# Performance work log

Measured on AMD Instinct MI355X. Metric: run time of the kernel, lower is better.

## Reference

```python
import jax, jax.numpy as jnp
import numpy as np

DIM = 1024
EXP = 4
B, S = 4, 4096


def setup_inputs() -> dict:
    key = jax.random.key(0)
    ks = jax.random.split(key, 20)
    d, h = DIM, DIM * EXP
    sc = 1.0 / np.sqrt(d)
    inp = {
        "x": jax.random.normal(ks[0], (B, S, d), dtype=jnp.float32),
        # attention linears, stored [in, out] so y = x @ W + b
        "wq": jax.random.normal(ks[1], (d, d), jnp.float32) * sc,
        "bq": jnp.zeros((d,), jnp.float32),
        "wk": jax.random.normal(ks[2], (d, d), jnp.float32) * sc,
        "bk": jnp.zeros((d,), jnp.float32),
        "wv": jax.random.normal(ks[3], (d, d), jnp.float32) * sc,
        "bv": jnp.zeros((d,), jnp.float32),
        "wo": jax.random.normal(ks[4], (d, d), jnp.float32) * sc,
        "bo": jnp.zeros((d,), jnp.float32),
        # FFN
        "w1": jax.random.normal(ks[5], (d, h), jnp.float32) * sc,
        "b1": jnp.zeros((h,), jnp.float32),
        "w2": jax.random.normal(ks[6], (h, d), jnp.float32) * (1.0 / np.sqrt(h)),
        "b2": jnp.zeros((d,), jnp.float32),
        # LayerNorms
        "g1": jnp.ones((d,), jnp.float32),
        "beta1": jnp.zeros((d,), jnp.float32),
        "g2": jnp.ones((d,), jnp.float32),
        "beta2": jnp.zeros((d,), jnp.float32),
    }
    return inp


def _layernorm(x, g, b, eps=1e-5):
    mu = jnp.mean(x, axis=-1, keepdims=True)
    var = jnp.mean(jnp.square(x - mu), axis=-1, keepdims=True)
    return (x - mu) * jax.lax.rsqrt(var + eps) * g + b


def _block(x, wq, bq, wk, bk, wv, bv, wo, bo, w1, b1, w2, b2, g1, beta1, g2, beta2):
    d = x.shape[-1]
    # attention sub-block (single head, full [B,S,S] scores as in source)
    h = _layernorm(x, g1, beta1)
    q = h @ wq + bq
    k = h @ wk + bk
    v = h @ wv + bv
    scores = jnp.einsum("bsd,btd->bst", q, k) / jnp.sqrt(jnp.asarray(d, x.dtype))
    attn = jax.nn.softmax(scores, axis=-1)
    a = jnp.einsum("bst,btd->bsd", attn, v) @ wo + bo
    x = x + a
    # FFN sub-block (exact GELU, matching torch nn.GELU default)
    h2 = _layernorm(x, g2, beta2)
    f = jax.nn.gelu(h2 @ w1 + b1, approximate=False) @ w2 + b2
    return x + f


def reference(x, wq, bq, wk, bk, wv, bv, wo, bo, w1, b1, w2, b2, g1, beta1, g2, beta2):
    return _block(x, wq, bq, wk, bk, wv, bv, wo, bo, w1, b1, w2, b2, g1, beta1, g2, beta2)
```

## Files before the change

### kernel.cpp

```cpp
#include <hip/hip_runtime.h>
#include <hip/hip_bf16.h>
#include <cstdint>

typedef __bf16 bf16;
typedef __bf16 bf16x8 __attribute__((ext_vector_type(8)));
typedef __bf16 bf16x4 __attribute__((ext_vector_type(4)));
typedef float f32x4 __attribute__((ext_vector_type(4)));

#define DEV __device__ __forceinline__

DEV float wred_sum(float v) {
#pragma unroll
  for (int off = 32; off > 0; off >>= 1) v += __shfl_xor(v, off, 64);
  return v;
}
DEV float wred_max(float v) {
#pragma unroll
  for (int off = 32; off > 0; off >>= 1) v = fmaxf(v, __shfl_xor(v, off, 64));
  return v;
}

__global__ void convT_kernel(const float* __restrict__ in, bf16* __restrict__ out,
                             int K, int N) {
  __shared__ float t[32][33];
  const int n0 = blockIdx.x * 32, k0 = blockIdx.y * 32;
  const int tx = threadIdx.x & 31, ty = threadIdx.x >> 5;
#pragma unroll
  for (int i = 0; i < 4; i++)
    t[ty + 8 * i][tx] = in[(long)(k0 + ty + 8 * i) * N + n0 + tx];
  __syncthreads();
#pragma unroll
  for (int i = 0; i < 4; i++)
    out[(long)(n0 + ty + 8 * i) * K + k0 + tx] = (bf16)t[tx][ty + 8 * i];
}

__global__ void transpose_bf16(const bf16* __restrict__ in, bf16* __restrict__ out,
                               int ldin, int ldout) {
  __shared__ bf16 t[32][33];
  const int c0 = blockIdx.x * 32, r0 = blockIdx.y * 32;
  const int tx = threadIdx.x & 31, ty = threadIdx.x >> 5;
#pragma unroll
  for (int i = 0; i < 4; i++)
    t[ty + 8 * i][tx] = in[(long)(r0 + ty + 8 * i) * ldin + c0 + tx];
  __syncthreads();
#pragma unroll
  for (int i = 0; i < 4; i++)
    out[(long)(c0 + ty + 8 * i) * ldout + r0 + tx] = t[tx][ty + 8 * i];
}

__global__ void ln_bf16_kernel(const float* __restrict__ x, const float* __restrict__ g,
                               const float* __restrict__ be, bf16* __restrict__ out) {
  const long row = blockIdx.x;
  const int tid = threadIdx.x;
  const float4 v = ((const float4*)(x + row * 1024))[tid];
  float s = v.x + v.y + v.z + v.w;
  float s2 = v.x * v.x + v.y * v.y + v.z * v.z + v.w * v.w;
  __shared__ float rs_[4], rs2_[4];
  s = wred_sum(s);
  s2 = wred_sum(s2);
  const int wave = tid >> 6, lane = tid & 63;
  if (lane == 0) { rs_[wave] = s; rs2_[wave] = s2; }
  __syncthreads();
  s = rs_[0] + rs_[1] + rs_[2] + rs_[3];
  s2 = rs2_[0] + rs2_[1] + rs2_[2] + rs2_[3];
  const float mu = s * (1.0f / 1024.0f);
  const float var = s2 * (1.0f / 1024.0f) - mu * mu;
  const float rstd = rsqrtf(var + 1e-5f);
  const float4 gg = ((const float4*)g)[tid];
  const float4 bb = ((const float4*)be)[tid];
  bf16x4 o;
  o[0] = (bf16)((v.x - mu) * rstd * gg.x + bb.x);
  o[1] = (bf16)((v.y - mu) * rstd * gg.y + bb.y);
  o[2] = (bf16)((v.z - mu) * rstd * gg.z + bb.z);
  o[3] = (bf16)((v.w - mu) * rstd * gg.w + bb.w);
  *(bf16x4*)(out + row * 1024 + tid * 4) = o;
}

__global__ void softmax_kernel(bf16* __restrict__ p) {
  const long row = blockIdx.x;
  bf16* pr = p + row * 4096;
  const int tid = threadIdx.x;
  bf16x8 a = *(const bf16x8*)(pr + tid * 16);
  bf16x8 b = *(const bf16x8*)(pr + tid * 16 + 8);
  float v[16];
#pragma unroll
  for (int i = 0; i < 8; i++) { v[i] = (float)a[i]; v[8 + i] = (float)b[i]; }
  float mx = -1e30f;
#pragma unroll
  for (int i = 0; i < 16; i++) mx = fmaxf(mx, v[i]);
  __shared__ float red1[4], red2[4];
  mx = wred_max(mx);
  const int wave = tid >> 6, lane = tid & 63;
  if (lane == 0) red1[wave] = mx;
  __syncthreads();
  mx = fmaxf(fmaxf(red1[0], red1[1]), fmaxf(red1[2], red1[3]));
  float s = 0.0f;
#pragma unroll
  for (int i = 0; i < 16; i++) { v[i] = __expf(v[i] - mx); s += v[i]; }
  s = wred_sum(s);
  if (lane == 0) red2[wave] = s;
  __syncthreads();
  s = red2[0] + red2[1] + red2[2] + red2[3];
  const float inv = 1.0f / s;
#pragma unroll
  for (int i = 0; i < 8; i++) { a[i] = (bf16)(v[i] * inv); b[i] = (bf16)(v[8 + i] * inv); }
  *(bf16x8*)(pr + tid * 16) = a;
  *(bf16x8*)(pr + tid * 16 + 8) = b;
}

enum { EPI_BF16 = 0, EPI_QKV = 1, EPI_GELU = 2, EPI_F32RES = 3 };

DEV void stage16(const bf16* g, bf16* l) {
  __builtin_amdgcn_global_load_lds((const __attribute__((address_space(1))) void*)g,
                                   (__attribute__((address_space(3))) void*)l, 16, 0, 0);
}

template <int EPI>
__global__ __launch_bounds__(256)
void gemm128(const bf16* __restrict__ A, const bf16* __restrict__ B,
             const float* __restrict__ bias, const float* __restrict__ resid,
             void* Cout, int M, int N, int K,
             int lda, int ldb, int ldc, float alpha) {
  extern __shared__ __align__(16) char smem[];
  bf16* sA = (bf16*)smem;
  bf16* sB = sA + 4 * 8192;
  int flat = (int)(blockIdx.y * gridDim.x + blockIdx.x);
  {
    const int nwg = (int)(gridDim.x * gridDim.y);
    const int qq = nwg >> 3, rr = nwg & 7;
    const int xcd = flat & 7, idx = flat >> 3;
    flat = (xcd < rr ? xcd * (qq + 1) : rr * (qq + 1) + (xcd - rr) * qq) + idx;
  }
  const int bix = flat % (int)gridDim.x, biy = flat / (int)gridDim.x;
  const int tid = threadIdx.x;
  const int lane = tid & 63;
  const int wid = tid >> 6;
  const int q = lane >> 4, r16 = lane & 15;
  const int wr = wid >> 1, wc = wid & 1;
  const long m0 = (long)biy * 128;
  const long n0 = (long)bix * 128;
  const int srow = tid >> 3;
  const int gcol = ((tid & 7) ^ (srow & 7)) * 8;
  const long lda32 = (long)lda * 32, ldb32 = (long)ldb * 32;
  const bf16* Ag = A + (m0 + srow) * (long)lda + gcol;
  const bf16* Bg = B + (n0 + srow) * (long)ldb + gcol;
  const int NT = K >> 6;
  const int swz = r16 * 64 + ((q ^ (r16 & 7)) * 8);
  const int abase = wr * 4096 + swz;
  const int bbase = wc * 4096 + swz;
  f32x4 acc[4][4] = {};

  const int PRE = NT < 3 ? NT : 3;
  for (int tt = 0; tt < PRE; ++tt) {
#pragma unroll
    for (int blk = 0; blk < 4; ++blk) {
      stage16(Ag + tt * 64 + blk * lda32, sA + tt * 8192 + tid * 8 + blk * 2048);
      stage16(Bg + tt * 64 + blk * ldb32, sB + tt * 8192 + tid * 8 + blk * 2048);
    }
  }
  if (NT >= 3)      asm volatile("s_waitcnt vmcnt(16)" ::: "memory");
  else if (NT == 2) asm volatile("s_waitcnt vmcnt(8)" ::: "memory");
  else              asm volatile("s_waitcnt vmcnt(0)" ::: "memory");
  __builtin_amdgcn_sched_barrier(0);
  __builtin_amdgcn_s_barrier();
  __builtin_amdgcn_sched_barrier(0);

  for (int t = 0; t < NT; ++t) {
    const int bx = (t & 3) * 8192;
    if (t + 3 < NT) {
      const int bs = ((t + 3) & 3) * 8192;
      const bf16* Agn = Ag + (t + 3) * 64;
      const bf16* Bgn = Bg + (t + 3) * 64;
#pragma unroll
      for (int blk = 0; blk < 4; ++blk) {
        stage16(Agn + blk * lda32, sA + bs + tid * 8 + blk * 2048);
        stage16(Bgn + blk * ldb32, sB + bs + tid * 8 + blk * 2048);
      }
    }
    const bf16* sAb = sA + bx;
    const bf16* sBb = sB + bx;
    bf16x8 a0[4], a1[4], b0[4], b1[4];
#pragma unroll
    for (int i = 0; i < 4; ++i) {
      a0[i] = *(const bf16x8*)(sAb + (abase + i * 1024));
      a1[i] = *(const bf16x8*)(sAb + ((abase + i * 1024) ^ 32));
      b0[i] = *(const bf16x8*)(sBb + (bbase + i * 1024));
      b1[i] = *(const bf16x8*)(sBb + ((bbase + i * 1024) ^ 32));
    }
#pragma unroll
    for (int i = 0; i < 4; ++i)
#pragma unroll
      for (int j = 0; j < 4; ++j) {
        acc[i][j] = __builtin_amdgcn_mfma_f32_16x16x32_bf16(b0[j], a0[i], acc[i][j], 0, 0, 0);
        acc[i][j] = __builtin_amdgcn_mfma_f32_16x16x32_bf16(b1[j], a1[i], acc[i][j], 0, 0, 0);
      }
    if (t + 3 < NT)      asm volatile("s_waitcnt vmcnt(16)" ::: "memory");
    else if (t + 2 < NT) asm volatile("s_waitcnt vmcnt(8)" ::: "memory");
    else if (t + 1 < NT) asm volatile("s_waitcnt vmcnt(0)" ::: "memory");
    if (t + 1 < NT) {
      __builtin_amdgcn_sched_barrier(0);
      __builtin_amdgcn_s_barrier();
      __builtin_amdgcn_sched_barrier(0);
    }
  }

#pragma unroll
  for (int i = 0; i < 4; ++i) {
    const long row = m0 + wr * 64 + i * 16 + r16;
#pragma unroll
    for (int j = 0; j < 4; ++j) {
      const int ncol = (int)n0 + wc * 64 + j * 16 + q * 4;
      float4 b4 = make_float4(0.f, 0.f, 0.f, 0.f);
      if (bias != nullptr) b4 = *(const float4*)(bias + ncol);
      float v0 = acc[i][j][0] * alpha + b4.x;
      float v1 = acc[i][j][1] * alpha + b4.y;
      float v2 = acc[i][j][2] * alpha + b4.z;
      float v3 = acc[i][j][3] * alpha + b4.w;
      if (EPI == EPI_F32RES) {
        const long idx = row * (long)ldc + ncol;
        const float4 rr = *(const float4*)(resid + idx);
        const float4 o = make_float4(v0 + rr.x, v1 + rr.y, v2 + rr.z, v3 + rr.w);
        *(float4*)((float*)Cout + idx) = o;
      } else {
        bf16x4 o;
        o[0] = (bf16)v0; o[1] = (bf16)v1; o[2] = (bf16)v2; o[3] = (bf16)v3;
        *(bf16x4*)((bf16*)Cout + row * (long)ldc + ncol) = o;
      }
    }
  }
}

template <int EPI>
__global__ __launch_bounds__(512, 2)
void gemm256(const bf16* __restrict__ A, const bf16* __restrict__ B,
             const float* __restrict__ bias, const float* bias2, const float* bias3,
             const float* resid, void* Cout, int M, int N, int K,
             int lda, int ldb, int ldc, float alpha) {
  extern __shared__ __align__(16) char smem[];
  bf16* sA = (bf16*)smem;
  bf16* sB = sA + 32768;
  const int tid = threadIdx.x;
  const int lane = tid & 63;
  const int wid = tid >> 6;
  const int q = lane >> 4, r16 = lane & 15;
  const int wr = wid >> 2, wc = wid & 3;
  const long m0 = (long)blockIdx.y * 256;
  const long n0 = (long)blockIdx.x * 256;
  const int srow = tid >> 3;
  const int gcol = ((tid & 7) ^ (srow & 7)) * 8;
  const long lda64 = (long)lda * 64, ldb64 = (long)ldb * 64;
  const bf16* AgT = A + (m0 + srow) * (long)lda + gcol;
  const bf16* BgT = B + (n0 + srow) * (long)ldb + gcol;
  bf16* lA = sA + tid * 8;
  bf16* lB = sB + tid * 8;
  const int NT = K >> 6;
  const int swz = r16 * 64 + ((q ^ (r16 & 7)) * 8);
  const int abase = wr * 8192 + swz;
  const int bbase = (wc >> 1) * 8192 + (wc & 1) * 4096 + swz;

  f32x4 acc[8][4] = {};

  stage16(AgT,              lA);
  stage16(AgT + 2 * lda64,  lA + 8192);
  stage16(AgT + lda64,      lA + 4096);
  stage16(AgT + 3 * lda64,  lA + 12288);
  stage16(BgT,              lB);
  stage16(BgT + ldb64,      lB + 4096);
  stage16(BgT + 2 * ldb64,  lB + 8192);
  stage16(BgT + 3 * ldb64,  lB + 12288);
  if (NT > 1) {
    stage16(AgT + 64,             lA + 16384);
    stage16(AgT + 64 + 2 * lda64, lA + 16384 + 8192);
    stage16(BgT + 64,             lB + 16384);
    stage16(BgT + 64 + ldb64,     lB + 16384 + 4096);
    stage16(BgT + 64 + 2 * ldb64, lB + 16384 + 8192);
    stage16(BgT + 64 + 3 * ldb64, lB + 16384 + 12288);
    stage16(AgT + 64 + lda64,     lA + 16384 + 4096);
    stage16(AgT + 64 + 3 * lda64, lA + 16384 + 12288);
    asm volatile("s_waitcnt vmcnt(8)" ::: "memory");
  } else {
    asm volatile("s_waitcnt vmcnt(0)" ::: "memory");
  }
  __builtin_amdgcn_sched_barrier(0);
  __builtin_amdgcn_s_barrier();
  __builtin_amdgcn_sched_barrier(0);

  for (int t = 0; t < NT; ++t) {
    const int bx = (t & 1) * 16384;
    const int nbx = 16384 - bx;
    const bf16* sAb = sA + bx;
    const bf16* sBb = sB + bx;
    const long k1 = (long)(t + 1) * 64;
    const long k2 = (long)(t + 2) * 64;
    bf16x8 b0[4], b1[4];
#pragma unroll
    for (int p = 0; p < 4; ++p) {
      if (p == 0) {
#pragma unroll
        for (int n = 0; n < 4; ++n) {
          b0[n] = *(const bf16x8*)(sBb + (bbase + n * 1024));
          b1[n] = *(const bf16x8*)(sBb + ((bbase + n * 1024) ^ 32));
        }
      }
      const int ab = abase + p * 2048;
      const bf16x8 a00 = *(const bf16x8*)(sAb + ab);
      const bf16x8 a10 = *(const bf16x8*)(sAb + (ab ^ 32));
      const bf16x8 a01 = *(const bf16x8*)(sAb + (ab + 1024));
      const bf16x8 a11 = *(const bf16x8*)(sAb + ((ab + 1024) ^ 32));
      if (p == 0 && t >= 1 && t + 1 < NT) {
        stage16(AgT + k1 + lda64,     lA + nbx + 4096);
        stage16(AgT + k1 + 3 * lda64, lA + nbx + 12288);
      }
      if (p == 1 && t + 2 < NT) {
        stage16(BgT + k2,         lB + bx);
        stage16(BgT + k2 + ldb64, lB + bx + 4096);
      }
      if (p == 2 && t + 2 < NT) {
        stage16(AgT + k2,             lA + bx);
        stage16(AgT + k2 + 2 * lda64, lA + bx + 8192);
      }
      if (p == 3 && t + 2 < NT) {
        stage16(BgT + k2 + 2 * ldb64, lB + bx + 8192);
        stage16(BgT + k2 + 3 * ldb64, lB + bx + 12288);
      }
      __builtin_amdgcn_sched_barrier(0);
      __builtin_amdgcn_s_barrier();
      __builtin_amdgcn_sched_barrier(0);
      __builtin_amdgcn_s_setprio(1);
#pragma unroll
      for (int n = 0; n < 4; ++n) {
        acc[2 * p][n]     = __builtin_amdgcn_mfma_f32_16x16x32_bf16(b0[n], a00, acc[2 * p][n], 0, 0, 0);
        acc[2 * p][n]     = __builtin_amdgcn_mfma_f32_16x16x32_bf16(b1[n], a10, acc[2 * p][n], 0, 0, 0);
        acc[2 * p + 1][n] = __builtin_amdgcn_mfma_f32_16x16x32_bf16(b0[n], a01, acc[2 * p + 1][n], 0, 0, 0);
        acc[2 * p + 1][n] = __builtin_amdgcn_mfma_f32_16x16x32_bf16(b1[n], a11, acc[2 * p + 1][n], 0, 0, 0);
      }
      __builtin_amdgcn_s_setprio(0);
      if (p == 1) {
        if (t + 2 < NT)      asm volatile("s_waitcnt vmcnt(10)" ::: "memory");
        else if (t + 1 < NT) asm volatile("s_waitcnt vmcnt(8)" ::: "memory");
        else                 asm volatile("s_waitcnt vmcnt(0)" ::: "memory");
      }
      if (p == 3) {
        if (t + 2 < NT)      asm volatile("s_waitcnt vmcnt(8)" ::: "memory");
        else if (t + 1 < NT) asm volatile("s_waitcnt vmcnt(2)" ::: "memory");
      }
      __builtin_amdgcn_sched_barrier(0);
      __builtin_amdgcn_s_barrier();
      __builtin_amdgcn_sched_barrier(0);
    }
  }

#pragma unroll
  for (int m = 0; m < 8; ++m) {
    const long row = m0 + wr * 128 + m * 16 + r16;
#pragma unroll
    for (int n = 0; n < 4; ++n) {
      const int ncol = (int)n0 + wc * 64 + n * 16 + q * 4;
      float4 b4 = make_float4(0.f, 0.f, 0.f, 0.f);
      if (EPI == EPI_QKV) {
        const int band = ncol >> 10;
        const float* bsel = band == 0 ? bias : (band == 1 ? bias2 : bias3);
        b4 = *(const float4*)(bsel + (ncol & 1023));
      } else if (bias != nullptr) {
        b4 = *(const float4*)(bias + ncol);
      }
      float v0 = acc[m][n][0] * alpha + b4.x;
      float v1 = acc[m][n][1] * alpha + b4.y;
      float v2 = acc[m][n][2] * alpha + b4.z;
      float v3 = acc[m][n][3] * alpha + b4.w;
      if (EPI == EPI_GELU) {
        v0 = 0.5f * v0 * (1.0f + erff(v0 * 0.70710678118654752f));
        v1 = 0.5f * v1 * (1.0f + erff(v1 * 0.70710678118654752f));
        v2 = 0.5f * v2 * (1.0f + erff(v2 * 0.70710678118654752f));
        v3 = 0.5f * v3 * (1.0f + erff(v3 * 0.70710678118654752f));
      }
      if (EPI == EPI_F32RES) {
        const long idx = row * (long)ldc + ncol;
        const float4 rr = *(const float4*)(resid + idx);
        const float4 o = make_float4(v0 + rr.x, v1 + rr.y, v2 + rr.z, v3 + rr.w);
        *(float4*)((float*)Cout + idx) = o;
      } else {
        bf16x4 o;
        o[0] = (bf16)v0; o[1] = (bf16)v1; o[2] = (bf16)v2; o[3] = (bf16)v3;
        *(bf16x4*)((bf16*)Cout + row * (long)ldc + ncol) = o;
      }
    }
  }
}

extern "C" void kernel_launch(void* const* d_in, const int* in_sizes, int n_in,
                              void* d_out, int out_size, void* d_ws, size_t ws_size,
                              hipStream_t stream) {
  const float* x  = (const float*)d_in[0];
  const float* wq = (const float*)d_in[1];
  const float* bq = (const float*)d_in[2];
  const float* wk = (const float*)d_in[3];
  const float* bk = (const float*)d_in[4];
  const float* wv = (const float*)d_in[5];
  const float* bv = (const float*)d_in[6];
  const float* wo = (const float*)d_in[7];
  const float* bo = (const float*)d_in[8];
  const float* w1 = (const float*)d_in[9];
  const float* b1 = (const float*)d_in[10];
  const float* w2 = (const float*)d_in[11];
  const float* b2 = (const float*)d_in[12];
  const float* g1 = (const float*)d_in[13];
  const float* be1 = (const float*)d_in[14];
  const float* g2 = (const float*)d_in[15];
  const float* be2 = (const float*)d_in[16];

  static int attr_done = 0;
  if (!attr_done) {
    attr_done = 1;
    hipFuncSetAttribute(reinterpret_cast<const void*>(&gemm256<EPI_QKV>),
                        hipFuncAttributeMaxDynamicSharedMemorySize, 131072);
    hipFuncSetAttribute(reinterpret_cast<const void*>(&gemm256<EPI_BF16>),
                        hipFuncAttributeMaxDynamicSharedMemorySize, 131072);
    hipFuncSetAttribute(reinterpret_cast<const void*>(&gemm256<EPI_GELU>),
                        hipFuncAttributeMaxDynamicSharedMemorySize, 131072);
    hipFuncSetAttribute(reinterpret_cast<const void*>(&gemm256<EPI_F32RES>),
                        hipFuncAttributeMaxDynamicSharedMemorySize, 131072);
    hipFuncSetAttribute(reinterpret_cast<const void*>(&gemm128<EPI_BF16>),
                        hipFuncAttributeMaxDynamicSharedMemorySize, 131072);
    hipFuncSetAttribute(reinterpret_cast<const void*>(&gemm128<EPI_F32RES>),
                        hipFuncAttributeMaxDynamicSharedMemorySize, 131072);
  }

  const long MB = 1 << 20;
  char* ws = (char*)d_ws;
  char* ob = (char*)d_out;
  bf16* WQKV = (bf16*)(ws + 0 * MB);
  bf16* WO   = (bf16*)(ws + 6 * MB);
  bf16* W1   = (bf16*)(ws + 8 * MB);
  bf16* W2   = (bf16*)(ws + 16 * MB);
  bf16* H    = (bf16*)(ws + 24 * MB);
  bf16* P    = (bf16*)(ob + 0 * MB);
  bf16* QKVb = (bf16*)(ob + 32 * MB);
  bf16* Vt   = (bf16*)(ob + 56 * MB);
  float* OUT = (float*)d_out;
  const dim3 blk(256);
  const dim3 blk512(512);
  const size_t SMEM = 131072;
  const size_t SMEM128 = 131072;

  convT_kernel<<<dim3(32, 32), blk, 0, stream>>>(wq, WQKV, 1024, 1024);
  convT_kernel<<<dim3(32, 32), blk, 0, stream>>>(wk, WQKV + 1024 * 1024, 1024, 1024);
  convT_kernel<<<dim3(32, 32), blk, 0, stream>>>(wv, WQKV + 2048 * 1024, 1024, 1024);
  convT_kernel<<<dim3(32, 32), blk, 0, stream>>>(wo, WO, 1024, 1024);
  convT_kernel<<<dim3(128, 32), blk, 0, stream>>>(w1, W1, 1024, 4096);
  convT_kernel<<<dim3(32, 128), blk, 0, stream>>>(w2, W2, 4096, 1024);
  ln_bf16_kernel<<<16384, blk, 0, stream>>>(x, g1, be1, H);
  for (int z = 0; z < 4; z++) {
    const long zo = (long)z * 4096 * 1024;
    gemm256<EPI_QKV><<<dim3(12, 16), blk512, SMEM, stream>>>(
        H + zo, WQKV, bq, bk, bv, nullptr, QKVb,
        4096, 3072, 1024, 1024, 1024, 3072, 1.0f);
    transpose_bf16<<<dim3(32, 128), blk, 0, stream>>>(QKVb + 2048, Vt, 3072, 4096);
    gemm256<EPI_BF16><<<dim3(16, 16), blk512, SMEM, stream>>>(
        QKVb, QKVb + 1024, nullptr, nullptr, nullptr, nullptr, P,
        4096, 4096, 1024, 3072, 3072, 4096, 1.0f / 32.0f);
    softmax_kernel<<<4096, blk, 0, stream>>>(P);
    gemm128<EPI_BF16><<<dim3(8, 32), blk, SMEM128, stream>>>(
        P, Vt, nullptr, nullptr, H + zo,
        4096, 1024, 4096, 4096, 4096, 1024, 1.0f);
  }
  gemm256<EPI_F32RES><<<dim3(4, 64), blk512, SMEM, stream>>>(
      H, WO, bo, nullptr, nullptr, x, OUT,
      16384, 1024, 1024, 1024, 1024, 1024, 1.0f);
  bf16* H2m = (bf16*)(ws + 0 * MB);
  bf16* Fm  = (bf16*)(ws + 24 * MB);
  for (int mc = 0; mc < 4; mc++) {
    const long ro = (long)mc * 4096 * 1024;
    ln_bf16_kernel<<<4096, blk, 0, stream>>>(OUT + ro, g2, be2, H2m);
    gemm256<EPI_GELU><<<dim3(16, 16), blk512, SMEM, stream>>>(
        H2m, W1, b1, nullptr, nullptr, nullptr, Fm,
        4096, 4096, 1024, 1024, 1024, 4096, 1.0f);
    gemm128<EPI_F32RES><<<dim3(8, 32), blk, SMEM128, stream>>>(
        Fm, W2, b2, OUT + ro, OUT + ro,
        4096, 1024, 4096, 4096, 4096, 1024, 1.0f);
  }
  (void)in_sizes; (void)n_in; (void)out_size; (void)ws_size;
}
```

Measured before the change: 1.257 ms.

## Replace 128x128 GEMM with 64x128 tile, 3-stage ring, two blocks per CU

The 128x128 GEMM used for attn@V and the FFN down-projection becomes a 64x128 tile kernel. It uses a 3-stage LDS ring instead of 4 stages, needs 72KB of shared memory, and sets launch bounds for 2 blocks per CU. The grid doubles to 512 blocks to improve CU fill for the K=4096, N=1024 GEMMs, and MFMA sections get setprio. The change also drops sched_barrier fences around s_barrier in gemm256, which gives the compiler more freedom but risks reordering around the LDS pipeline.

```diff
diff --git a/kernel.cpp b/kernel.cpp
--- a/kernel.cpp
+++ b/kernel.cpp
@@ -115,29 +115,30 @@
                                    (__attribute__((address_space(3))) void*)l, 16, 0, 0);
 }
 
+DEV int xcd_swizzle(int flat, int nwg) {
+  const int qq = nwg >> 3, rr = nwg & 7;
+  const int xcd = flat & 7, idx = flat >> 3;
+  return (xcd < rr ? xcd * (qq + 1) : rr * (qq + 1) + (xcd - rr) * qq) + idx;
+}
+
 template <int EPI>
-__global__ __launch_bounds__(256)
-void gemm128(const bf16* __restrict__ A, const bf16* __restrict__ B,
-             const float* __restrict__ bias, const float* __restrict__ resid,
-             void* Cout, int M, int N, int K,
-             int lda, int ldb, int ldc, float alpha) {
+__global__ __launch_bounds__(256, 2)
+void gemm64(const bf16* __restrict__ A, const bf16* __restrict__ B,
+            const float* __restrict__ bias, const float* __restrict__ resid,
+            void* Cout, int M, int N, int K,
+            int lda, int ldb, int ldc, float alpha) {
   extern __shared__ __align__(16) char smem[];
   bf16* sA = (bf16*)smem;
-  bf16* sB = sA + 4 * 8192;
+  bf16* sB = sA + 3 * 4096;
   int flat = (int)(blockIdx.y * gridDim.x + blockIdx.x);
-  {
-    const int nwg = (int)(gridDim.x * gridDim.y);
-    const int qq = nwg >> 3, rr = nwg & 7;
-    const int xcd = flat & 7, idx = flat >> 3;
-    flat = (xcd < rr ? xcd * (qq + 1) : rr * (qq + 1) + (xcd - rr) * qq) + idx;
-  }
+  flat = xcd_swizzle(flat, (int)(gridDim.x * gridDim.y));
   const int bix = flat % (int)gridDim.x, biy = flat / (int)gridDim.x;
   const int tid = threadIdx.x;
   const int lane = tid & 63;
   const int wid = tid >> 6;
   const int q = lane >> 4, r16 = lane & 15;
   const int wr = wid >> 1, wc = wid & 1;
-  const long m0 = (long)biy * 128;
+  const long m0 = (long)biy * 64;
   const long n0 = (long)bix * 128;
   const int srow = tid >> 3;
   const int gcol = ((tid & 7) ^ (srow & 7)) * 8;
@@ -146,67 +147,70 @@
   const bf16* Bg = B + (n0 + srow) * (long)ldb + gcol;
   const int NT = K >> 6;
   const int swz = r16 * 64 + ((q ^ (r16 & 7)) * 8);
-  const int abase = wr * 4096 + swz;
+  const int abase = wr * 2048 + swz;
   const int bbase = wc * 4096 + swz;
-  f32x4 acc[4][4] = {};
-
-  const int PRE = NT < 3 ? NT : 3;
+  f32x4 acc[2][4] = {};
+
+  const int PRE = NT < 2 ? NT : 2;
   for (int tt = 0; tt < PRE; ++tt) {
 #pragma unroll
-    for (int blk = 0; blk < 4; ++blk) {
-      stage16(Ag + tt * 64 + blk * lda32, sA + tt * 8192 + tid * 8 + blk * 2048);
+    for (int blk = 0; blk < 2; ++blk)
+      stage16(Ag + tt * 64 + blk * lda32, sA + tt * 4096 + tid * 8 + blk * 2048);
+#pragma unroll
+    for (int blk = 0; blk < 4; ++blk)
       stage16(Bg + tt * 64 + blk * ldb32, sB + tt * 8192 + tid * 8 + blk * 2048);
-    }
-  }
-  if (NT >= 3)      asm volatile("s_waitcnt vmcnt(16)" ::: "memory");
-  else if (NT == 2) asm volatile("s_waitcnt vmcnt(8)" ::: "memory");
-  else              asm volatile("s_waitcnt vmcnt(0)" ::: "memory");
-  __builtin_amdgcn_sched_barrier(0);
+  }
+  if (NT >= 2) asm volatile("s_waitcnt vmcnt(6)" ::: "memory");
+  else         asm volatile("s_waitcnt vmcnt(0)" ::: "memory");
   __builtin_amdgcn_s_barrier();
-  __builtin_amdgcn_sched_barrier(0);
-
+
+  int bxA = 0, bxB = 0;
+  int bsA = 8192, bsB = 16384;
   for (int t = 0; t < NT; ++t) {
-    const int bx = (t & 3) * 8192;
-    if (t + 3 < NT) {
-      const int bs = ((t + 3) & 3) * 8192;
-      const bf16* Agn = Ag + (t + 3) * 64;
-      const bf16* Bgn = Bg + (t + 3) * 64;
-#pragma unroll
-      for (int blk = 0; blk < 4; ++blk) {
-        stage16(Agn + blk * lda32, sA + bs + tid * 8 + blk * 2048);
-        stage16(Bgn + blk * ldb32, sB + bs + tid * 8 + blk * 2048);
-      }
-    }
-    const bf16* sAb = sA + bx;
-    const bf16* sBb = sB + bx;
-    bf16x8 a0[4], a1[4], b0[4], b1[4];
-#pragma unroll
-    for (int i = 0; i < 4; ++i) {
+    if (t + 2 < NT) {
+      const bf16* Agn = Ag + (t + 2) * 64;
+      const bf16* Bgn = Bg + (t + 2) * 64;
+#pragma unroll
+      for (int blk = 0; blk < 2; ++blk)
+        stage16(Agn + blk * lda32, sA + bsA + tid * 8 + blk * 2048);
+#pragma unroll
+      for (int blk = 0; blk < 4; ++blk)
+        stage16(Bgn + blk * ldb32, sB + bsB + tid * 8 + blk * 2048);
+    }
+    const bf16* sAb = sA + bxA;
+    const bf16* sBb = sB + bxB;
+    bf16x8 a0[2], a1[2], b0[4], b1[4];
+#pragma unroll
+    for (int i = 0; i < 2; ++i) {
       a0[i] = *(const bf16x8*)(sAb + (abase + i * 1024));
       a1[i] = *(const bf16x8*)(sAb + ((abase + i * 1024) ^ 32));
-      b0[i] = *(const bf16x8*)(sBb + (bbase + i * 1024));
-      b1[i] = *(const bf16x8*)(sBb + ((bbase + i * 1024) ^ 32));
-    }
-#pragma unroll
-    for (int i = 0; i < 4; ++i)
+    }
+#pragma unroll
+    for (int j = 0; j < 4; ++j) {
+      b0[j] = *(const bf16x8*)(sBb + (bbase + j * 1024));
+      b1[j] = *(const bf16x8*)(sBb + ((bbase + j * 1024) ^ 32));
+    }
+    __builtin_amdgcn_s_setprio(1);
+#pragma unroll
+    for (int i = 0; i < 2; ++i)
 #pragma unroll
       for (int j = 0; j < 4; ++j) {
         acc[i][j] = __builtin_amdgcn_mfma_f32_16x16x32_bf16(b0[j], a0[i], acc[i][j], 0, 0, 0);
         acc[i][j] = __builtin_amdgcn_mfma_f32_16x16x32_bf16(b1[j], a1[i], acc[i][j], 0, 0, 0);
       }
-    if (t + 3 < NT)      asm volatile("s_waitcnt vmcnt(16)" ::: "memory");
-    else if (t + 2 < NT) asm volatile("s_waitcnt vmcnt(8)" ::: "memory");
+    __builtin_amdgcn_s_setprio(0);
+    if (t + 2 < NT)      asm volatile("s_waitcnt vmcnt(6)" ::: "memory");
     else if (t + 1 < NT) asm volatile("s_waitcnt vmcnt(0)" ::: "memory");
-    if (t + 1 < NT) {
-      __builtin_amdgcn_sched_barrier(0);
-      __builtin_amdgcn_s_barrier();
-      __builtin_amdgcn_sched_barrier(0);
-    }
-  }
-
-#pragma unroll
-  for (int i = 0; i < 4; ++i) {
-    const long row = m0 + wr * 64 + i * 16 + r16;
+    if (t + 1 < NT) __builtin_amdgcn_s_barrier();
+    bxA += 4096; if (bxA == 12288) bxA = 0;
+    bxB += 8192; if (bxB == 24576) bxB = 0;
+    bsA += 4096; if (bsA == 12288) bsA = 0;
+    bsB += 8192; if (bsB == 24576) bsB = 0;
+  }
+
+#pragma unroll
+  for (int i = 0; i < 2; ++i) {
+    const long row = m0 + wr * 32 + i * 16 + r16;
 #pragma unroll
     for (int j = 0; j < 4; ++j) {
       const int ncol = (int)n0 + wc * 64 + j * 16 + q * 4;
@@ -281,9 +285,7 @@
   } else {
     asm volatile("s_waitcnt vmcnt(0)" ::: "memory");
   }
-  __builtin_amdgcn_sched_barrier(0);
   __builtin_amdgcn_s_barrier();
-  __builtin_amdgcn_sched_barrier(0);
 
   for (int t = 0; t < NT; ++t) {
     const int bx = (t & 1) * 16384;
@@ -323,9 +325,7 @@
         stage16(BgT + k2 + 2 * ldb64, lB + bx + 8192);
         stage16(BgT + k2 + 3 * ldb64, lB + bx + 12288);
       }
-      __builtin_amdgcn_sched_barrier(0);
       __builtin_amdgcn_s_barrier();
-      __builtin_amdgcn_sched_barrier(0);
       __builtin_amdgcn_s_setprio(1);
 #pragma unroll
       for (int n = 0; n < 4; ++n) {
@@ -344,9 +344,7 @@
         if (t + 2 < NT)      asm volatile("s_waitcnt vmcnt(8)" ::: "memory");
         else if (t + 1 < NT) asm volatile("s_waitcnt vmcnt(2)" ::: "memory");
       }
-      __builtin_amdgcn_sched_barrier(0);
       __builtin_amdgcn_s_barrier();
-      __builtin_amdgcn_sched_barrier(0);
     }
   }
 
@@ -420,10 +418,10 @@
                         hipFuncAttributeMaxDynamicSharedMemorySize, 131072);
     hipFuncSetAttribute(reinterpret_cast<const void*>(&gemm256<EPI_F32RES>),
                         hipFuncAttributeMaxDynamicSharedMemorySize, 131072);
-    hipFuncSetAttribute(reinterpret_cast<const void*>(&gemm128<EPI_BF16>),
-                        hipFuncAttributeMaxDynamicSharedMemorySize, 131072);
-    hipFuncSetAttribute(reinterpret_cast<const void*>(&gemm128<EPI_F32RES>),
-                        hipFuncAttributeMaxDynamicSharedMemorySize, 131072);
+    hipFuncSetAttribute(reinterpret_cast<const void*>(&gemm64<EPI_BF16>),
+                        hipFuncAttributeMaxDynamicSharedMemorySize, 73728);
+    hipFuncSetAttribute(reinterpret_cast<const void*>(&gemm64<EPI_F32RES>),
+                        hipFuncAttributeMaxDynamicSharedMemorySize, 73728);
   }
 
   const long MB = 1 << 20;
@@ -441,7 +439,7 @@
   const dim3 blk(256);
   const dim3 blk512(512);
   const size_t SMEM = 131072;
-  const size_t SMEM128 = 131072;
+  const size_t SMEM64 = 73728;
 
   convT_kernel<<<dim3(32, 32), blk, 0, stream>>>(wq, WQKV, 1024, 1024);
   convT_kernel<<<dim3(32, 32), blk, 0, stream>>>(wk, WQKV + 1024 * 1024, 1024, 1024);
@@ -460,7 +458,7 @@
         QKVb, QKVb + 1024, nullptr, nullptr, nullptr, nullptr, P,
         4096, 4096, 1024, 3072, 3072, 4096, 1.0f / 32.0f);
     softmax_kernel<<<4096, blk, 0, stream>>>(P);
-    gemm128<EPI_BF16><<<dim3(8, 32), blk, SMEM128, stream>>>(
+    gemm64<EPI_BF16><<<dim3(8, 64), blk, SMEM64, stream>>>(
         P, Vt, nullptr, nullptr, H + zo,
         4096, 1024, 4096, 4096, 4096, 1024, 1.0f);
   }
@@ -475,7 +473,7 @@
     gemm256<EPI_GELU><<<dim3(16, 16), blk512, SMEM, stream>>>(
         H2m, W1, b1, nullptr, nullptr, nullptr, Fm,
         4096, 4096, 1024, 1024, 1024, 4096, 1.0f);
-    gemm128<EPI_F32RES><<<dim3(8, 32), blk, SMEM128, stream>>>(
+    gemm64<EPI_F32RES><<<dim3(8, 64), blk, SMEM64, stream>>>(
         Fm, W2, b2, OUT + ro, OUT + ro,
         4096, 1024, 4096, 4096, 4096, 1024, 1.0f);
   }
```

Result: faster. 1.199 ms (-4.6%).
